# Optimization experiments

Measured on AMD Instinct MI355X. Metric: run time of the kernel, lower is better.

The kernel has to match this reference:

```python
import jax, jax.numpy as jnp
import numpy as np

B, S, D = 8, 2048, 1024
NEG = jnp.float32(-(2.0**32) + 1.0)

def setup_inputs() -> dict:
    key = jax.random.key(0)
    ks = jax.random.split(key, 7)
    s = 1.0 / np.sqrt(D)
    return {
        "x": jax.random.normal(ks[0], (B, S, D), dtype=jnp.float32),
        "Wq": jax.random.normal(ks[1], (D, D), dtype=jnp.float32) * s,
        "bq": jnp.zeros((D,), dtype=jnp.float32),
        "Wk": jax.random.normal(ks[2], (D, D), dtype=jnp.float32) * s,
        "bk": jnp.zeros((D,), dtype=jnp.float32),
        "Wv": jax.random.normal(ks[3], (D, D), dtype=jnp.float32) * s,
        "bv": jnp.zeros((D,), dtype=jnp.float32),
    }

def reference(x, Wq, bq, Wk, bk, Wv, bv):
    # QKV projections with inline ReLU
    q = jax.nn.relu(jnp.einsum('bsd,df->bsf', x, Wq) + bq)
    k = jax.nn.relu(jnp.einsum('bsd,df->bsf', x, Wk) + bk)
    v = jax.nn.relu(jnp.einsum('bsd,df->bsf', x, Wv) + bv)
    # scaled scores [B, S, S]
    scores = jnp.einsum('bqd,bkd->bqk', q, k) / jnp.sqrt(jnp.float32(D))
    # sin-based key/query masks derived from token sums [B, S]
    masks = jnp.sin(jnp.abs(jnp.sum(x, axis=-1)))
    # mask keys where mask == 0
    scores = jnp.where(masks[:, None, :] == 0, NEG, scores)
    attn = jax.nn.softmax(scores, axis=-1)
    # post-softmax query masking (broadcast over keys)
    attn = attn * masks[:, :, None]
    out = jnp.einsum('bqk,bkd->bqd', attn, v) + q  # residual add of q
    return out
```

## Files before the change

### kernel.cpp

```cpp
#include <hip/hip_runtime.h>

#define DEV __device__ __forceinline__

typedef __attribute__((ext_vector_type(8))) short bf16x8;
typedef __attribute__((ext_vector_type(4))) float f32x4;

static constexpr int Bn = 8;
static constexpr int Sn = 2048;
static constexpr int Dn = 1024;
static constexpr int Mtot = Bn * Sn;

static constexpr int ABUF = 8192;
static constexpr int TBUF = 12288;

DEV void gload_lds16(const void* g, void* l) {
  __builtin_amdgcn_global_load_lds(
      (const __attribute__((address_space(1))) void*)g,
      (__attribute__((address_space(3))) void*)l, 16, 0, 0);
}

DEV float bf2f(unsigned short u) {
  union { unsigned int i; float f; } c;
  c.i = ((unsigned int)u) << 16;
  return c.f;
}
DEV unsigned short f2bf(float f) {
  union { float f; unsigned int i; } c;
  c.f = f;
  unsigned int lsb = (c.i >> 16) & 1u;
  return (unsigned short)((c.i + 0x7fffu + lsb) >> 16);
}

__global__ __launch_bounds__(256) void prep_kernel(const float* __restrict__ x,
                                                   unsigned short* __restrict__ xbf,
                                                   float* __restrict__ masks) {
  const int w = threadIdx.x >> 6, l = threadIdx.x & 63;
  const int row = blockIdx.x * 4 + w;
  const float* xr = x + (size_t)row * Dn;
  unsigned short* xo = xbf + (size_t)row * Dn;
  float s = 0.f;
  #pragma unroll
  for (int i = 0; i < 4; i++) {
    float4 v = ((const float4*)xr)[i * 64 + l];
    s += (v.x + v.y) + (v.z + v.w);
    unsigned int p0 = (unsigned int)f2bf(v.x) | ((unsigned int)f2bf(v.y) << 16);
    unsigned int p1 = (unsigned int)f2bf(v.z) | ((unsigned int)f2bf(v.w) << 16);
    *(uint2*)&xo[i * 256 + l * 4] = make_uint2(p0, p1);
  }
  #pragma unroll
  for (int off = 32; off > 0; off >>= 1) s += __shfl_xor(s, off);
  if (l == 0) masks[row] = sinf(fabsf(s));
}

__global__ __launch_bounds__(256) void wt_kernel(const float* __restrict__ Wq,
                                                 const float* __restrict__ Wk,
                                                 const float* __restrict__ Wv,
                                                 unsigned short* __restrict__ Wt) {
  const float* W = blockIdx.z == 0 ? Wq : (blockIdx.z == 1 ? Wk : Wv);
  unsigned short* out = Wt + (size_t)blockIdx.z * Dn * Dn;
  __shared__ float tile[32][33];
  const int r0 = blockIdx.y * 32, c0 = blockIdx.x * 32;
  const int t = threadIdx.x;
  {
    const int r = t >> 3, c4 = (t & 7) * 4;
    float4 v = *(const float4*)&W[(size_t)(r0 + r) * Dn + c0 + c4];
    tile[r][c4 + 0] = v.x; tile[r][c4 + 1] = v.y;
    tile[r][c4 + 2] = v.z; tile[r][c4 + 3] = v.w;
  }
  __syncthreads();
  {
    const int f = t >> 3, d4 = (t & 7) * 4;
    unsigned short o[4];
    #pragma unroll
    for (int i = 0; i < 4; i++) o[i] = f2bf(tile[d4 + i][f]);
    unsigned int p0 = (unsigned int)o[0] | ((unsigned int)o[1] << 16);
    unsigned int p1 = (unsigned int)o[2] | ((unsigned int)o[3] << 16);
    *(uint2*)&out[(size_t)(c0 + f) * Dn + r0 + d4] = make_uint2(p0, p1);
  }
}

DEV void gemmtile(const unsigned short* __restrict__ Ag, int lda,
                  const unsigned short* __restrict__ Bg, int ldb,
                  int K, unsigned short* lds, f32x4 acc[4][4]) {
  const int tid = threadIdx.x;
  const int l = tid & 63, w = tid >> 6;
  const int wr = w >> 1, wc = w & 1;
  const int lr = l & 15, lk = l >> 4;

  #pragma unroll
  for (int mi = 0; mi < 4; mi++)
    #pragma unroll
    for (int ni = 0; ni < 4; ni++)
      #pragma unroll
      for (int q = 0; q < 4; q++) acc[mi][ni][q] = 0.f;

  int offA[4], offB[4];
  #pragma unroll
  for (int mi = 0; mi < 4; mi++) {
    const int row = wr * 64 + mi * 16 + lr;
    offA[mi] = (row * 4 + (lk ^ ((row >> 1) & 3))) * 8;
  }
  #pragma unroll
  for (int ni = 0; ni < 4; ni++) {
    const int row = wc * 64 + ni * 16 + lr;
    offB[ni] = (row * 4 + (lk ^ ((row >> 1) & 3))) * 8;
  }
  int sA[2], dA[2], sB, dB;
  #pragma unroll
  for (int i = 0; i < 2; i++) {
    const int ci = i * 512 + tid;
    const int row = ci >> 2, c = (ci & 3) ^ ((row >> 1) & 3);
    sA[i] = row * lda + c * 8;
    dA[i] = ci * 8;
  }
  {
    const int ci = tid;
    const int row = ci >> 2, c = (ci & 3) ^ ((row >> 1) & 3);
    sB = row * ldb + c * 8;
    dB = ci * 8;
  }

  const int NT = K >> 5;
  unsigned short* bc = lds;
  unsigned short* b1 = lds + TBUF;
  unsigned short* b2 = lds + 2 * TBUF;

  #pragma unroll
  for (int t = 0; t < 2; t++) {
    unsigned short* bf = lds + t * TBUF;
    gload_lds16(Ag + sA[0] + t * 32, bf + dA[0]);
    gload_lds16(Ag + sA[1] + t * 32, bf + dA[1]);
    gload_lds16(Bg + sB + t * 32, bf + ABUF + dB);
  }
  asm volatile("s_waitcnt vmcnt(3)\n\ts_barrier" ::: "memory");

  for (int t = 0; t < NT; t++) {
    const bool st = (t + 2 < NT);
    const int kt = (t + 2) * 32;

    bf16x8 af[4], bv[4];
    #pragma unroll
    for (int mi = 0; mi < 4; mi++) af[mi] = *(const bf16x8*)(bc + offA[mi]);
    #pragma unroll
    for (int ni = 0; ni < 4; ni++) bv[ni] = *(const bf16x8*)(bc + ABUF + offB[ni]);

    if (st) {
      gload_lds16(Ag + sA[0] + kt, b2 + dA[0]);
      gload_lds16(Ag + sA[1] + kt, b2 + dA[1]);
    }
    __builtin_amdgcn_s_setprio(1);
    #pragma unroll
    for (int mi = 0; mi < 4; mi++) {
      acc[mi][0] = __builtin_amdgcn_mfma_f32_16x16x32_bf16(af[mi], bv[0], acc[mi][0], 0, 0, 0);
      acc[mi][1] = __builtin_amdgcn_mfma_f32_16x16x32_bf16(af[mi], bv[1], acc[mi][1], 0, 0, 0);
    }
    __builtin_amdgcn_s_setprio(0);
    if (st) {
      gload_lds16(Bg + sB + kt, b2 + ABUF + dB);
    }
    __builtin_amdgcn_s_setprio(1);
    #pragma unroll
    for (int mi = 0; mi < 4; mi++) {
      acc[mi][2] = __builtin_amdgcn_mfma_f32_16x16x32_bf16(af[mi], bv[2], acc[mi][2], 0, 0, 0);
      acc[mi][3] = __builtin_amdgcn_mfma_f32_16x16x32_bf16(af[mi], bv[3], acc[mi][3], 0, 0, 0);
    }
    __builtin_amdgcn_s_setprio(0);

    if (t + 2 < NT) {
      asm volatile("s_waitcnt vmcnt(3)\n\ts_barrier" ::: "memory");
    } else if (t + 1 < NT) {
      asm volatile("s_waitcnt vmcnt(0)\n\ts_barrier" ::: "memory");
    }
    unsigned short* tmp = bc; bc = b1; b1 = b2; b2 = tmp;
  }
}

__global__ __launch_bounds__(512, 4) void qkv_kernel(
    const unsigned short* __restrict__ xbf, const unsigned short* __restrict__ Wt,
    const float* __restrict__ bq, const float* __restrict__ bk,
    const float* __restrict__ bv,
    unsigned short* __restrict__ qo, unsigned short* __restrict__ ko,
    unsigned short* __restrict__ vT) {
  __shared__ __align__(16) unsigned short lds[3 * TBUF];
  const int orig = blockIdx.x;
  const int wg = (orig & 7) * 192 + (orig >> 3);
  const int which = wg >> 9;
  const int rem = wg & 511;
  const int m0 = (rem >> 3) * 256, n0 = (rem & 7) * 128;
  const unsigned short* Ag = xbf + (size_t)m0 * Dn;
  const unsigned short* Bg = Wt + (size_t)which * Dn * Dn + (size_t)n0 * Dn;
  f32x4 acc[4][4];
  gemmtile(Ag, Dn, Bg, Dn, Dn, lds, acc);

  const float* bias = which == 0 ? bq : (which == 1 ? bk : bv);
  const int tid = threadIdx.x;
  const int l = tid & 63, w = tid >> 6;
  const int wr = w >> 1, wc = w & 1;
  const int lr = l & 15, lk = l >> 4;

  if (which < 2) {
    unsigned short* out = which == 0 ? qo : ko;
    #pragma unroll
    for (int mi = 0; mi < 4; mi++) {
      #pragma unroll
      for (int ni = 0; ni < 4; ni++) {
        const int col = n0 + wc * 64 + ni * 16 + lr;
        const float bcol = bias[col];
        #pragma unroll
        for (int j = 0; j < 4; j++) {
          const int row = m0 + wr * 64 + mi * 16 + lk * 4 + j;
          out[(size_t)row * Dn + col] = f2bf(fmaxf(acc[mi][ni][j] + bcol, 0.f));
        }
      }
    }
  } else {
    const int b = m0 >> 11;
    const int s0g = m0 & (Sn - 1);
    __syncthreads();
    #pragma unroll
    for (int mi = 0; mi < 4; mi++) {
      const int sc = wr * 16 + mi * 4 + lk;
      #pragma unroll
      for (int ni = 0; ni < 4; ni++) {
        const int d = wc * 64 + ni * 16 + lr;
        const float bcol = bias[n0 + d];
        unsigned short o0 = f2bf(fmaxf(acc[mi][ni][0] + bcol, 0.f));
        unsigned short o1 = f2bf(fmaxf(acc[mi][ni][1] + bcol, 0.f));
        unsigned short o2 = f2bf(fmaxf(acc[mi][ni][2] + bcol, 0.f));
        unsigned short o3 = f2bf(fmaxf(acc[mi][ni][3] + bcol, 0.f));
        const int scp = sc ^ (d & 63);
        *(uint2*)&lds[d * 256 + scp * 4] =
            make_uint2((unsigned int)o0 | ((unsigned int)o1 << 16),
                       (unsigned int)o2 | ((unsigned int)o3 << 16));
      }
    }
    __syncthreads();
    #pragma unroll
    for (int it = 0; it < 16; it++) {
      const int lin = it * 512 + tid;
      const int d = lin >> 6, sc = lin & 63;
      const int scp = sc ^ (d & 63);
      uint2 v = *(const uint2*)&lds[d * 256 + scp * 4];
      *(uint2*)&vT[((size_t)b * Dn + n0 + d) * Sn + s0g + sc * 4] = v;
    }
  }
}

__global__ __launch_bounds__(512, 4) void scores_kernel(
    const unsigned short* __restrict__ qbf, const unsigned short* __restrict__ kbf,
    const float* __restrict__ masks, unsigned short* __restrict__ P,
    float* __restrict__ lpart) {
  __shared__ __align__(16) unsigned short lds[3 * TBUF];
  const int orig = blockIdx.x;
  const int wg = (orig & 7) * 128 + (orig >> 3);
  const int b = wg >> 7;
  const int rem = wg & 127;
  const int m0 = (rem >> 4) * 256, n0 = (rem & 15) * 128;
  const unsigned short* Ag = qbf + ((size_t)b * Sn + m0) * Dn;
  const unsigned short* Bg = kbf + ((size_t)b * Sn + n0) * Dn;
  f32x4 acc[4][4];
  gemmtile(Ag, Dn, Bg, Dn, Dn, lds, acc);

  const int tid = threadIdx.x;
  const int l = tid & 63, w = tid >> 6;
  const int wr = w >> 1, wc = w & 1;
  const int lr = l & 15, lk = l >> 4;

  __syncthreads();
  float* psum = (float*)lds;

  float mkv[4];
  #pragma unroll
  for (int ni = 0; ni < 4; ni++) mkv[ni] = masks[b * Sn + n0 + wc * 64 + ni * 16 + lr];

  unsigned short* Pb = P + (size_t)b * Sn * Sn;
  #pragma unroll
  for (int mi = 0; mi < 4; mi++) {
    #pragma unroll
    for (int j = 0; j < 4; j++) {
      const int rloc = wr * 64 + mi * 16 + lk * 4 + j;
      const size_t rbase = (size_t)(m0 + rloc) * Sn;
      float rsum = 0.f;
      #pragma unroll
      for (int ni = 0; ni < 4; ni++) {
        const int col = n0 + wc * 64 + ni * 16 + lr;
        const float p = (mkv[ni] == 0.f) ? 0.f : __expf(acc[mi][ni][j] * 0.03125f);
        const unsigned short pq = f2bf(p);
        Pb[rbase + col] = pq;
        rsum += bf2f(pq);
      }
      rsum += __shfl_xor(rsum, 1); rsum += __shfl_xor(rsum, 2);
      rsum += __shfl_xor(rsum, 4); rsum += __shfl_xor(rsum, 8);
      if (lr == 0) psum[wc * 256 + rloc] = rsum;
    }
  }
  __syncthreads();
  if (tid < 256) {
    const float v = psum[tid] + psum[256 + tid];
    lpart[((size_t)b * Sn + m0 + tid) * 16 + (rem & 15)] = v;
  }
}

__global__ __launch_bounds__(256) void reduce_kernel(const float* __restrict__ lpart,
                                                     const float* __restrict__ masks,
                                                     float* __restrict__ scale) {
  const int r = blockIdx.x * 256 + threadIdx.x;
  const float4* p = (const float4*)(lpart + (size_t)r * 16);
  float4 a = p[0], b = p[1], c = p[2], d = p[3];
  const float sum = ((a.x + a.y) + (a.z + a.w)) + ((b.x + b.y) + (b.z + b.w)) +
                    ((c.x + c.y) + (c.z + c.w)) + ((d.x + d.y) + (d.z + d.w));
  scale[r] = masks[r] / sum;
}

__global__ __launch_bounds__(512, 4) void pv_kernel(
    const unsigned short* __restrict__ P, const unsigned short* __restrict__ vT,
    const float* __restrict__ scale, const unsigned short* __restrict__ qbf,
    float* __restrict__ out) {
  __shared__ __align__(16) unsigned short lds[3 * TBUF];
  const int orig = blockIdx.x;
  const int wg = (orig & 7) * 64 + (orig >> 3);
  const int b = wg >> 6;
  const int rem = wg & 63;
  const int m0 = (rem >> 3) * 256, n0 = (rem & 7) * 128;
  const unsigned short* Ag = P + (size_t)b * Sn * Sn + (size_t)m0 * Sn;
  const unsigned short* Bg = vT + (size_t)b * Dn * Sn + (size_t)n0 * Sn;
  f32x4 acc[4][4];
  gemmtile(Ag, Sn, Bg, Sn, Sn, lds, acc);

  const int tid = threadIdx.x;
  const int l = tid & 63, w = tid >> 6;
  const int wr = w >> 1, wc = w & 1;
  const int lr = l & 15, lk = l >> 4;
  #pragma unroll
  for (int mi = 0; mi < 4; mi++) {
    #pragma unroll
    for (int j = 0; j < 4; j++) {
      const int row = m0 + wr * 64 + mi * 16 + lk * 4 + j;
      const float sc = scale[b * Sn + row];
      const size_t rbase = ((size_t)b * Sn + row) * Dn;
      #pragma unroll
      for (int ni = 0; ni < 4; ni++) {
        const int col = n0 + wc * 64 + ni * 16 + lr;
        out[rbase + col] = acc[mi][ni][j] * sc + bf2f(qbf[rbase + col]);
      }
    }
  }
}

extern "C" void kernel_launch(void* const* d_in, const int* in_sizes, int n_in,
                              void* d_out, int out_size, void* d_ws, size_t ws_size,
                              hipStream_t stream) {
  const float* x  = (const float*)d_in[0];
  const float* Wq = (const float*)d_in[1];
  const float* bq = (const float*)d_in[2];
  const float* Wk = (const float*)d_in[3];
  const float* bk = (const float*)d_in[4];
  const float* Wv = (const float*)d_in[5];
  const float* bv = (const float*)d_in[6];
  float* out = (float*)d_out;

  char* ws = (char*)d_ws;
  size_t off = 0;
  auto alloc = [&](size_t bytes) {
    char* p = ws + off;
    off += (bytes + 255) & ~(size_t)255;
    return p;
  };
  unsigned short* xbf = (unsigned short*)alloc((size_t)Mtot * Dn * 2);
  unsigned short* qbf = (unsigned short*)alloc((size_t)Mtot * Dn * 2);
  unsigned short* kbf = (unsigned short*)alloc((size_t)Mtot * Dn * 2);
  unsigned short* vT  = (unsigned short*)alloc((size_t)Bn * Dn * Sn * 2);
  unsigned short* P   = (unsigned short*)alloc((size_t)Bn * Sn * Sn * 2);
  unsigned short* Wt  = (unsigned short*)alloc((size_t)3 * Dn * Dn * 2);
  float* masks = (float*)alloc((size_t)Mtot * 4);
  float* lpart = (float*)alloc((size_t)Mtot * 16 * 4);
  float* scale = (float*)alloc((size_t)Mtot * 4);

  prep_kernel<<<Mtot / 4, 256, 0, stream>>>(x, xbf, masks);
  wt_kernel<<<dim3(32, 32, 3), 256, 0, stream>>>(Wq, Wk, Wv, Wt);
  qkv_kernel<<<1536, 512, 0, stream>>>(xbf, Wt, bq, bk, bv, qbf, kbf, vT);
  scores_kernel<<<1024, 512, 0, stream>>>(qbf, kbf, masks, P, lpart);
  reduce_kernel<<<Mtot / 256, 256, 0, stream>>>(lpart, masks, scale);
  pv_kernel<<<512, 512, 0, stream>>>(P, vT, scale, qbf, out);
}
```

Before: 285.9 us.

## Use 256x256 tiles with 4-stage LDS pipeline for scores and PV GEMMs

Adds a new GEMM tile routine with 256x256 output tiles per 512-thread block, 8x4 MFMA accumulators per wave and a 4-deep LDS ring buffer with new swizzling. The scores and PV kernels use it, which halves their grid sizes, and the row-sum partials shrink from 16 to 8 per row. The goal is to raise data reuse per byte loaded and hide more load latency. The cost is more registers and LDS per block, lower occupancy, and fewer blocks to fill the GPU.

```diff
diff --git a/kernel.cpp b/kernel.cpp
--- a/kernel.cpp
+++ b/kernel.cpp
@@ -12,6 +12,8 @@
 
 static constexpr int ABUF = 8192;
 static constexpr int TBUF = 12288;
+static constexpr int BUFS_A = 16384;
+static constexpr int BHALF_A = 8192;
 
 DEV void gload_lds16(const void* g, void* l) {
   __builtin_amdgcn_global_load_lds(
@@ -79,9 +81,9 @@
   }
 }
 
-DEV void gemmtile(const unsigned short* __restrict__ Ag, int lda,
-                  const unsigned short* __restrict__ Bg, int ldb,
-                  int K, unsigned short* lds, f32x4 acc[4][4]) {
+DEV void gemmB(const unsigned short* __restrict__ Ag, int lda,
+               const unsigned short* __restrict__ Bg, int ldb,
+               int K, unsigned short* lds, f32x4 acc[4][4]) {
   const int tid = threadIdx.x;
   const int l = tid & 63, w = tid >> 6;
   const int wr = w >> 1, wc = w & 1;
@@ -175,10 +177,106 @@
   }
 }
 
+DEV void gemmA(const unsigned short* __restrict__ Ag, int lda,
+               const unsigned short* __restrict__ Bg, int ldb,
+               int K, unsigned short* lds, f32x4 acc[8][4]) {
+  const int tid = threadIdx.x;
+  const int l = tid & 63, w = tid >> 6;
+  const int wr = w >> 2, wc = w & 3;
+  const int lr = l & 15, lk = l >> 4;
+
+  #pragma unroll
+  for (int mi = 0; mi < 8; mi++)
+    #pragma unroll
+    for (int ni = 0; ni < 4; ni++)
+      #pragma unroll
+      for (int q = 0; q < 4; q++) acc[mi][ni][q] = 0.f;
+
+  int offA[8], offB[4];
+  #pragma unroll
+  for (int mi = 0; mi < 8; mi++) {
+    const int row = wr * 128 + mi * 16 + lr;
+    const int L = row >> 1, p = ((row & 1) * 4 + lk) ^ (L & 7);
+    offA[mi] = L * 64 + p * 8;
+  }
+  #pragma unroll
+  for (int ni = 0; ni < 4; ni++) {
+    const int row = wc * 64 + ni * 16 + lr;
+    const int L = row >> 1, p = ((row & 1) * 4 + lk) ^ (L & 7);
+    offB[ni] = L * 64 + p * 8;
+  }
+  int sA[2], sB[2], dO[2];
+  #pragma unroll
+  for (int i = 0; i < 2; i++) {
+    const int ci = i * 512 + tid;
+    const int L = ci >> 3, p = ci & 7, e = p ^ (L & 7);
+    const int grow = 2 * L + (e >> 2), gkc = e & 3;
+    sA[i] = grow * lda + gkc * 8;
+    sB[i] = grow * ldb + gkc * 8;
+    dO[i] = ci * 8;
+  }
+
+  const int NT = K >> 5;
+  #pragma unroll
+  for (int t = 0; t < 3; t++) {
+    unsigned short* bf = lds + t * BUFS_A;
+    gload_lds16(Ag + sA[0] + t * 32, bf + dO[0]);
+    gload_lds16(Ag + sA[1] + t * 32, bf + dO[1]);
+    gload_lds16(Bg + sB[0] + t * 32, bf + BHALF_A + dO[0]);
+    gload_lds16(Bg + sB[1] + t * 32, bf + BHALF_A + dO[1]);
+  }
+  asm volatile("s_waitcnt vmcnt(8)\n\ts_barrier" ::: "memory");
+
+  for (int t = 0; t < NT; t++) {
+    unsigned short* bufc = lds + (t & 3) * BUFS_A;
+    unsigned short* bufs = lds + ((t + 3) & 3) * BUFS_A;
+    const bool st = (t + 3 < NT);
+    const int kt = (t + 3) * 32;
+
+    bf16x8 af[8], bv[4];
+    #pragma unroll
+    for (int mi = 0; mi < 8; mi++) af[mi] = *(const bf16x8*)(bufc + offA[mi]);
+    bv[0] = *(const bf16x8*)(bufc + BHALF_A + offB[0]);
+    bv[1] = *(const bf16x8*)(bufc + BHALF_A + offB[1]);
+    if (st) {
+      gload_lds16(Ag + sA[0] + kt, bufs + dO[0]);
+      gload_lds16(Ag + sA[1] + kt, bufs + dO[1]);
+    }
+    __builtin_amdgcn_s_setprio(1);
+    #pragma unroll
+    for (int mi = 0; mi < 8; mi++) {
+      acc[mi][0] = __builtin_amdgcn_mfma_f32_16x16x32_bf16(af[mi], bv[0], acc[mi][0], 0, 0, 0);
+      acc[mi][1] = __builtin_amdgcn_mfma_f32_16x16x32_bf16(af[mi], bv[1], acc[mi][1], 0, 0, 0);
+    }
+    __builtin_amdgcn_s_setprio(0);
+    bv[2] = *(const bf16x8*)(bufc + BHALF_A + offB[2]);
+    bv[3] = *(const bf16x8*)(bufc + BHALF_A + offB[3]);
+    if (st) {
+      gload_lds16(Bg + sB[0] + kt, bufs + BHALF_A + dO[0]);
+      gload_lds16(Bg + sB[1] + kt, bufs + BHALF_A + dO[1]);
+    }
+    __builtin_amdgcn_s_setprio(1);
+    #pragma unroll
+    for (int mi = 0; mi < 8; mi++) {
+      acc[mi][2] = __builtin_amdgcn_mfma_f32_16x16x32_bf16(af[mi], bv[2], acc[mi][2], 0, 0, 0);
+      acc[mi][3] = __builtin_amdgcn_mfma_f32_16x16x32_bf16(af[mi], bv[3], acc[mi][3], 0, 0, 0);
+    }
+    __builtin_amdgcn_s_setprio(0);
+
+    if (t < NT - 3) {
+      asm volatile("s_waitcnt vmcnt(8)\n\ts_barrier" ::: "memory");
+    } else if (t == NT - 3) {
+      asm volatile("s_waitcnt vmcnt(4)\n\ts_barrier" ::: "memory");
+    } else if (t == NT - 2) {
+      asm volatile("s_waitcnt vmcnt(0)\n\ts_barrier" ::: "memory");
+    }
+  }
+}
+
 __global__ __launch_bounds__(512, 4) void qkv_kernel(
     const unsigned short* __restrict__ xbf, const unsigned short* __restrict__ Wt,
     const float* __restrict__ bq, const float* __restrict__ bk,
-    const float* __restrict__ bv,
+    const float* __restrict__ bv_,
     unsigned short* __restrict__ qo, unsigned short* __restrict__ ko,
     unsigned short* __restrict__ vT) {
   __shared__ __align__(16) unsigned short lds[3 * TBUF];
@@ -190,9 +288,9 @@
   const unsigned short* Ag = xbf + (size_t)m0 * Dn;
   const unsigned short* Bg = Wt + (size_t)which * Dn * Dn + (size_t)n0 * Dn;
   f32x4 acc[4][4];
-  gemmtile(Ag, Dn, Bg, Dn, Dn, lds, acc);
-
-  const float* bias = which == 0 ? bq : (which == 1 ? bk : bv);
+  gemmB(Ag, Dn, Bg, Dn, Dn, lds, acc);
+
+  const float* bias = which == 0 ? bq : (which == 1 ? bk : bv_);
   const int tid = threadIdx.x;
   const int l = tid & 63, w = tid >> 6;
   const int wr = w >> 1, wc = w & 1;
@@ -246,24 +344,24 @@
   }
 }
 
-__global__ __launch_bounds__(512, 4) void scores_kernel(
+__global__ __launch_bounds__(512, 2) void scores_kernel(
     const unsigned short* __restrict__ qbf, const unsigned short* __restrict__ kbf,
     const float* __restrict__ masks, unsigned short* __restrict__ P,
     float* __restrict__ lpart) {
-  __shared__ __align__(16) unsigned short lds[3 * TBUF];
+  __shared__ __align__(16) unsigned short lds[4 * BUFS_A];
   const int orig = blockIdx.x;
-  const int wg = (orig & 7) * 128 + (orig >> 3);
-  const int b = wg >> 7;
-  const int rem = wg & 127;
-  const int m0 = (rem >> 4) * 256, n0 = (rem & 15) * 128;
+  const int wg = (orig & 7) * 64 + (orig >> 3);
+  const int b = wg >> 6;
+  const int rem = wg & 63;
+  const int m0 = (rem >> 3) * 256, n0 = (rem & 7) * 256;
   const unsigned short* Ag = qbf + ((size_t)b * Sn + m0) * Dn;
   const unsigned short* Bg = kbf + ((size_t)b * Sn + n0) * Dn;
-  f32x4 acc[4][4];
-  gemmtile(Ag, Dn, Bg, Dn, Dn, lds, acc);
+  f32x4 acc[8][4];
+  gemmA(Ag, Dn, Bg, Dn, Dn, lds, acc);
 
   const int tid = threadIdx.x;
   const int l = tid & 63, w = tid >> 6;
-  const int wr = w >> 1, wc = w & 1;
+  const int wr = w >> 2, wc = w & 3;
   const int lr = l & 15, lk = l >> 4;
 
   __syncthreads();
@@ -275,10 +373,10 @@
 
   unsigned short* Pb = P + (size_t)b * Sn * Sn;
   #pragma unroll
-  for (int mi = 0; mi < 4; mi++) {
+  for (int mi = 0; mi < 8; mi++) {
     #pragma unroll
     for (int j = 0; j < 4; j++) {
-      const int rloc = wr * 64 + mi * 16 + lk * 4 + j;
+      const int rloc = wr * 128 + mi * 16 + lk * 4 + j;
       const size_t rbase = (size_t)(m0 + rloc) * Sn;
       float rsum = 0.f;
       #pragma unroll
@@ -296,8 +394,8 @@
   }
   __syncthreads();
   if (tid < 256) {
-    const float v = psum[tid] + psum[256 + tid];
-    lpart[((size_t)b * Sn + m0 + tid) * 16 + (rem & 15)] = v;
+    const float v = psum[tid] + psum[256 + tid] + psum[512 + tid] + psum[768 + tid];
+    lpart[((size_t)b * Sn + m0 + tid) * 8 + (rem & 7)] = v;
   }
 }
 
@@ -305,37 +403,36 @@
                                                      const float* __restrict__ masks,
                                                      float* __restrict__ scale) {
   const int r = blockIdx.x * 256 + threadIdx.x;
-  const float4* p = (const float4*)(lpart + (size_t)r * 16);
-  float4 a = p[0], b = p[1], c = p[2], d = p[3];
-  const float sum = ((a.x + a.y) + (a.z + a.w)) + ((b.x + b.y) + (b.z + b.w)) +
-                    ((c.x + c.y) + (c.z + c.w)) + ((d.x + d.y) + (d.z + d.w));
+  const float4* p = (const float4*)(lpart + (size_t)r * 8);
+  float4 a = p[0], b = p[1];
+  const float sum = ((a.x + a.y) + (a.z + a.w)) + ((b.x + b.y) + (b.z + b.w));
   scale[r] = masks[r] / sum;
 }
 
-__global__ __launch_bounds__(512, 4) void pv_kernel(
+__global__ __launch_bounds__(512, 2) void pv_kernel(
     const unsigned short* __restrict__ P, const unsigned short* __restrict__ vT,
     const float* __restrict__ scale, const unsigned short* __restrict__ qbf,
     float* __restrict__ out) {
-  __shared__ __align__(16) unsigned short lds[3 * TBUF];
+  __shared__ __align__(16) unsigned short lds[4 * BUFS_A];
   const int orig = blockIdx.x;
-  const int wg = (orig & 7) * 64 + (orig >> 3);
-  const int b = wg >> 6;
-  const int rem = wg & 63;
-  const int m0 = (rem >> 3) * 256, n0 = (rem & 7) * 128;
+  const int wg = (orig & 7) * 32 + (orig >> 3);
+  const int b = wg >> 5;
+  const int rem = wg & 31;
+  const int m0 = (rem >> 2) * 256, n0 = (rem & 3) * 256;
   const unsigned short* Ag = P + (size_t)b * Sn * Sn + (size_t)m0 * Sn;
   const unsigned short* Bg = vT + (size_t)b * Dn * Sn + (size_t)n0 * Sn;
-  f32x4 acc[4][4];
-  gemmtile(Ag, Sn, Bg, Sn, Sn, lds, acc);
+  f32x4 acc[8][4];
+  gemmA(Ag, Sn, Bg, Sn, Sn, lds, acc);
 
   const int tid = threadIdx.x;
   const int l = tid & 63, w = tid >> 6;
-  const int wr = w >> 1, wc = w & 1;
+  const int wr = w >> 2, wc = w & 3;
   const int lr = l & 15, lk = l >> 4;
   #pragma unroll
-  for (int mi = 0; mi < 4; mi++) {
+  for (int mi = 0; mi < 8; mi++) {
     #pragma unroll
     for (int j = 0; j < 4; j++) {
-      const int row = m0 + wr * 64 + mi * 16 + lk * 4 + j;
+      const int row = m0 + wr * 128 + mi * 16 + lk * 4 + j;
       const float sc = scale[b * Sn + row];
       const size_t rbase = ((size_t)b * Sn + row) * Dn;
       #pragma unroll
@@ -373,13 +470,13 @@
   unsigned short* P   = (unsigned short*)alloc((size_t)Bn * Sn * Sn * 2);
   unsigned short* Wt  = (unsigned short*)alloc((size_t)3 * Dn * Dn * 2);
   float* masks = (float*)alloc((size_t)Mtot * 4);
-  float* lpart = (float*)alloc((size_t)Mtot * 16 * 4);
+  float* lpart = (float*)alloc((size_t)Mtot * 8 * 4);
   float* scale = (float*)alloc((size_t)Mtot * 4);
 
   prep_kernel<<<Mtot / 4, 256, 0, stream>>>(x, xbf, masks);
   wt_kernel<<<dim3(32, 32, 3), 256, 0, stream>>>(Wq, Wk, Wv, Wt);
   qkv_kernel<<<1536, 512, 0, stream>>>(xbf, Wt, bq, bk, bv, qbf, kbf, vT);
-  scores_kernel<<<1024, 512, 0, stream>>>(qbf, kbf, masks, P, lpart);
+  scores_kernel<<<512, 512, 0, stream>>>(qbf, kbf, masks, P, lpart);
   reduce_kernel<<<Mtot / 256, 256, 0, stream>>>(lpart, masks, scale);
-  pv_kernel<<<512, 512, 0, stream>>>(P, vT, scale, qbf, out);
-}
+  pv_kernel<<<256, 512, 0, stream>>>(P, vT, scale, qbf, out);
+}
```

Result: faster. 277.4 us (-3.0%).
